# Performance work log

Hardware: AMD Instinct MI355X
Metric: run time of the kernel (lower is better)

Reference implementation:

```python
import jax, jax.numpy as jnp
from jax import lax
import numpy as np

B, N, S, K = 8, 4096, 1024, 32
D_FEAT = 64
EPS = 1e-5


def fps_idx(pts, npoint):
    # pts: [N,3] -> farthest point sampling indices [npoint] (deterministic start at 0)
    n = pts.shape[0]
    def body(i, state):
        dist, far, idxs = state
        idxs = idxs.at[i].set(far)
        d = jnp.sum((pts - pts[far]) ** 2, axis=-1)
        dist = jnp.minimum(dist, d)
        return dist, jnp.argmax(dist).astype(jnp.int32), idxs
    init = (jnp.full((n,), 1e10, pts.dtype), jnp.int32(0), jnp.zeros((npoint,), jnp.int32))
    _, _, idxs = lax.fori_loop(0, npoint, body, init)
    return idxs


def bn(x, g, b, axes, c_axis):
    # batch-norm, training mode (batch statistics), matching torch default module state
    m = jnp.mean(x, axes, keepdims=True)
    v = jnp.var(x, axes, keepdims=True)
    shape = [1] * x.ndim
    shape[c_axis] = -1
    return g.reshape(shape) * (x - m) * lax.rsqrt(v + EPS) + b.reshape(shape)


def conv1x1(x, w, b):
    # x: [B,C,S,K], w: [O,C], b: [O]
    return jnp.einsum('oc,bcsk->bosk', w, x) + b[None, :, None, None]


def setup_inputs():
    key = jax.random.key(0)
    ks = jax.random.split(key, 20)
    p = lambda k, shape: jax.random.normal(k, shape, jnp.float32) * 0.05
    inp = {
        'xyz': jax.random.normal(ks[0], (B, 3, N), jnp.float32),
        'features': jax.random.normal(ks[1], (B, D_FEAT, N), jnp.float32),
        # main MLP: 67 -> 64 -> 64 -> 128
        'w0': p(ks[2], (64, 67)), 'b0': p(ks[3], (64,)), 'g0': jnp.ones(64), 'be0': jnp.zeros(64),
        'w1': p(ks[4], (64, 64)), 'b1': p(ks[5], (64,)), 'g1': jnp.ones(64), 'be1': jnp.zeros(64),
        'w2': p(ks[6], (128, 64)), 'b2': p(ks[7], (128,)), 'g2': jnp.ones(128), 'be2': jnp.zeros(128),
        # WeightNet: 3 -> 8 -> 8 -> 16
        'ww0': p(ks[8], (8, 3)), 'wb0': p(ks[9], (8,)), 'wg0': jnp.ones(8), 'wbe0': jnp.zeros(8),
        'ww1': p(ks[10], (8, 8)), 'wb1': p(ks[11], (8,)), 'wg1': jnp.ones(8), 'wbe1': jnp.zeros(8),
        'ww2': p(ks[12], (16, 8)), 'wb2': p(ks[13], (16,)), 'wg2': jnp.ones(16), 'wbe2': jnp.zeros(16),
        # final linear 16*128 -> 128 and BN1d
        'lw': p(ks[14], (128, 16 * 128)), 'lb': p(ks[15], (128,)),
        'lg': jnp.ones(128), 'lbe': jnp.zeros(128),
    }
    return inp


def reference(xyz, features, w0, b0, g0, be0, w1, b1, g1, be1, w2, b2, g2, be2,
              ww0, wb0, wg0, wbe0, ww1, wb1, wg1, wbe1, ww2, wb2, wg2, wbe2,
              lw, lb, lg, lbe):
    xyz_t = jnp.transpose(xyz, (0, 2, 1))          # [B,N,3]
    feat_t = jnp.transpose(features, (0, 2, 1))    # [B,N,D]

    # farthest point sampling (indices non-differentiable, as in CUDA FPS)
    fidx = jax.vmap(lambda pts: fps_idx(pts, S))(lax.stop_gradient(xyz_t))  # [B,S]
    fps_xyz = jnp.take_along_axis(xyz_t, fidx[..., None], axis=1)           # [B,S,3]

    # KNN: squared distances [B,S,N], take K smallest
    d2 = (jnp.sum(fps_xyz ** 2, -1, keepdims=True)
          + jnp.sum(xyz_t ** 2, -1)[:, None, :]
          - 2.0 * jnp.einsum('bsc,bnc->bsn', fps_xyz, xyz_t))
    _, idx = lax.top_k(-lax.stop_gradient(d2), K)                            # [B,S,K]

    gather = jax.vmap(lambda src, i: src[i])
    grouped_xyz = gather(xyz_t, idx) - fps_xyz[:, :, None, :]                # [B,S,K,3]
    grouped_feat = gather(feat_t, idx)                                       # [B,S,K,D]
    nf = jnp.concatenate([grouped_xyz, grouped_feat], axis=-1)               # [B,S,K,3+D]

    nf = jnp.transpose(nf, (0, 3, 1, 2))                                     # [B,C,S,K]
    for w, b, g, be in ((w0, b0, g0, be0), (w1, b1, g1, be1), (w2, b2, g2, be2)):
        nf = jax.nn.relu(bn(conv1x1(nf, w, b), g, be, (0, 2, 3), 1))

    gx = jnp.transpose(grouped_xyz, (0, 3, 1, 2))                            # [B,3,S,K]
    wts = gx
    for w, b, g, be in ((ww0, wb0, wg0, wbe0), (ww1, wb1, wg1, wbe1), (ww2, wb2, wg2, wbe2)):
        wts = jax.nn.relu(bn(conv1x1(wts, w, b), g, be, (0, 2, 3), 1))       # [B,16,S,K]

    agg = jnp.einsum('bdsk,bcsk->bsdc', nf, wts)                             # [B,S,128,16]
    agg = agg.reshape(agg.shape[0], agg.shape[1], -1)                        # [B,S,2048] (D outer, C inner)
    lin = agg @ lw.T + lb                                                    # [B,S,128]
    lin = jnp.transpose(lin, (0, 2, 1))                                      # [B,128,S]
    out_f = jax.nn.relu(bn(lin, lg, lbe, (0, 2), 1))

    new_xyz = jnp.transpose(fps_xyz, (0, 2, 1))                              # [B,3,S]
    return (new_xyz, out_f)
```

## Files before the change

### kernel.cpp

```cpp
#include <hip/hip_runtime.h>
#include <hip/hip_bf16.h>

#define BB 8
#define NN 4096
#define SS 1024
#define KK 32
#define PP (BB*SS*KK)

typedef unsigned long long u64;
typedef unsigned int u32;
typedef unsigned short u16;
typedef float f32x2 __attribute__((ext_vector_type(2)));
typedef float f32x4 __attribute__((ext_vector_type(4)));
typedef short bf16x8 __attribute__((ext_vector_type(8)));

#define ST_Y0 0
#define ST_W0 64
#define ST_Y1 72
#define ST_W1 136
#define ST_Y2 144
#define ST_W2 272
#define ST_LIN 288

static __device__ __forceinline__ float bf2f(u32 u){ return __uint_as_float(u<<16); }
static __device__ __forceinline__ u16 f2bf(float f){ u32 u=__float_as_uint(f); return (u16)((u + 0x7FFFu + ((u>>16)&1u))>>16); }

static __device__ __forceinline__ f32x2 pk_add(f32x2 a, f32x2 b){
  f32x2 d; asm("v_pk_add_f32 %0, %1, %2" : "=v"(d) : "v"(a), "v"(b)); return d;
}
static __device__ __forceinline__ f32x2 pk_mul(f32x2 a, f32x2 b){
  f32x2 d; asm("v_pk_mul_f32 %0, %1, %2" : "=v"(d) : "v"(a), "v"(b)); return d;
}

static __device__ __forceinline__ f32x4 mfma16(bf16x8 a, bf16x8 b, f32x4 c){
  return __builtin_amdgcn_mfma_f32_16x16x32_bf16(a,b,c,0,0,0);
}

static __device__ __forceinline__ uint4 pack8(const float* v){
  uint4 r;
  r.x=(u32)f2bf(v[0])|((u32)f2bf(v[1])<<16);
  r.y=(u32)f2bf(v[2])|((u32)f2bf(v[3])<<16);
  r.z=(u32)f2bf(v[4])|((u32)f2bf(v[5])<<16);
  r.w=(u32)f2bf(v[6])|((u32)f2bf(v[7])<<16);
  return r;
}

static __device__ __forceinline__ void unp8_aff(uint4 r, const float* A, const float* C, int cb, float* o){
  o[0]=fmaxf(fmaf(bf2f(r.x&0xffffu),A[cb+0],C[cb+0]),0.f);
  o[1]=fmaxf(fmaf(bf2f(r.x>>16)    ,A[cb+1],C[cb+1]),0.f);
  o[2]=fmaxf(fmaf(bf2f(r.y&0xffffu),A[cb+2],C[cb+2]),0.f);
  o[3]=fmaxf(fmaf(bf2f(r.y>>16)    ,A[cb+3],C[cb+3]),0.f);
  o[4]=fmaxf(fmaf(bf2f(r.z&0xffffu),A[cb+4],C[cb+4]),0.f);
  o[5]=fmaxf(fmaf(bf2f(r.z>>16)    ,A[cb+5],C[cb+5]),0.f);
  o[6]=fmaxf(fmaf(bf2f(r.w&0xffffu),A[cb+6],C[cb+6]),0.f);
  o[7]=fmaxf(fmaf(bf2f(r.w>>16)    ,A[cb+7],C[cb+7]),0.f);
}

template<int CTRL, int RMASK>
static __device__ __forceinline__ u32 dppmax(u32 m){
  u32 t=(u32)__builtin_amdgcn_update_dpp(0, (int)m, CTRL, RMASK, 0xf, false);
  return t>m ? t : m;
}
template<int CTRL, int RMASK>
static __device__ __forceinline__ float dppadd1(float v){
  float t=__uint_as_float((u32)__builtin_amdgcn_update_dpp(0,(int)__float_as_uint(v),CTRL,RMASK,0xf,false));
  return v+t;
}
static __device__ __forceinline__ float dppsum(float v){
  v=dppadd1<0x111,0xf>(v);
  v=dppadd1<0x112,0xf>(v);
  v=dppadd1<0x114,0xf>(v);
  v=dppadd1<0x118,0xf>(v);
  v=dppadd1<0x142,0xa>(v);
  v=dppadd1<0x143,0xc>(v);
  return v;
}
static __device__ __forceinline__ float rl63(float v){
  return __uint_as_float((u32)__builtin_amdgcn_readlane((int)__float_as_uint(v),63));
}

__global__ __launch_bounds__(256) void k_featT(const float* __restrict__ f, float* __restrict__ ft,
    const float* __restrict__ ww0,const float* __restrict__ ww1,const float* __restrict__ ww2,
    const float* __restrict__ lw, u16* __restrict__ lwbf,
    float* __restrict__ wt0,float* __restrict__ wt1,float* __restrict__ wt2,
    float* __restrict__ statsf){
  __shared__ float tile[64][65];
  if (blockIdx.x==512){
    int t=threadIdx.x;
    for (int i=t;i<1024;i+=256) statsf[i]=0.f;
    for (int i=t;i<8*3;i+=256){ int o=i/3,k=i%3; wt0[k*8+o]=ww0[i]; }
    for (int i=t;i<8*8;i+=256){ int o=i>>3,k=i&7; wt1[k*8+o]=ww1[i]; }
    for (int i=t;i<16*8;i+=256){ int o=i>>3,k=i&7; wt2[k*16+o]=ww2[i]; }
    return;
  }
  {
    int base2=blockIdx.x*512;
    for (int i=threadIdx.x;i<512;i+=256) lwbf[base2+i]=f2bf(lw[base2+i]);
  }
  int b=blockIdx.x>>6; int n0=(blockIdx.x&63)*64;
  const float* fb=f+(size_t)b*64*NN;
  int c0=threadIdx.x>>6, nn=threadIdx.x&63;
  #pragma unroll
  for (int it=0;it<16;it++){ int c=c0+it*4; tile[c][nn]=fb[(size_t)c*NN+n0+nn]; }
  __syncthreads();
  int cc=threadIdx.x&63, n1=threadIdx.x>>6;
  float* fo=ft+((size_t)b*NN+n0)*64;
  #pragma unroll
  for (int it=0;it<16;it++){ int n=n1+it*4; fo[(size_t)n*64+cc]=tile[cc][n]; }
}

__global__ __launch_bounds__(512) void k_fps(const float* __restrict__ xyz,
                                             float* __restrict__ fpsq, float* __restrict__ outx){
  __shared__ float X[NN], Y[NN], Z[NN];
  __shared__ float QX[SS], QY[SS], QZ[SS];
  __shared__ u64 red[2][8];
  int b=blockIdx.x, t=threadIdx.x;
  const float* xb=xyz+(size_t)b*3*NN;
  for (int i=t;i<NN;i+=512){ X[i]=xb[i]; Y[i]=xb[NN+i]; Z[i]=xb[2*NN+i]; }
  __syncthreads();
  f32x2 px[4],py[4],pz[4],dd[4];
  #pragma unroll
  for (int k=0;k<4;k++){
    int i=t*8+2*k;
    px[k].x=X[i]; px[k].y=X[i+1];
    py[k].x=Y[i]; py[k].y=Y[i+1];
    pz[k].x=Z[i]; pz[k].y=Z[i+1];
    dd[k].x=1e10f; dd[k].y=1e10f;
  }
  int wv=t>>6, ln=t&63;
  int far=0;
  for (int s=0;s<SS;s++){
    float fx=X[far], fy=Y[far], fz=Z[far];
    if (t==0){ QX[s]=fx; QY[s]=fy; QZ[s]=fz; }
    f32x2 nfx, nfy, nfz;
    nfx.x=-fx; nfx.y=-fx; nfy.x=-fy; nfy.y=-fy; nfz.x=-fz; nfz.y=-fz;
    #pragma unroll
    for (int k=0;k<4;k++){
      f32x2 dx=pk_add(px[k],nfx);
      f32x2 xx=pk_mul(dx,dx);
      f32x2 dy=pk_add(py[k],nfy);
      f32x2 yy=pk_mul(dy,dy);
      f32x2 dz=pk_add(pz[k],nfz);
      f32x2 zz=pk_mul(dz,dz);
      f32x2 s1=pk_add(xx,yy);
      f32x2 d2=pk_add(s1,zz);
      dd[k].x=fminf(dd[k].x,d2.x);
      dd[k].y=fminf(dd[k].y,d2.y);
    }
    float m01=fmaxf(dd[0].x,dd[0].y), m23=fmaxf(dd[1].x,dd[1].y);
    float m45=fmaxf(dd[2].x,dd[2].y), m67=fmaxf(dd[3].x,dd[3].y);
    u32 m=__float_as_uint(fmaxf(fmaxf(m01,m23),fmaxf(m45,m67)));
    m=dppmax<0x111,0xf>(m);
    m=dppmax<0x112,0xf>(m);
    m=dppmax<0x114,0xf>(m);
    m=dppmax<0x118,0xf>(m);
    u32 r15=(u32)__builtin_amdgcn_readlane((int)m,15);
    u32 r31=(u32)__builtin_amdgcn_readlane((int)m,31);
    u32 r47=(u32)__builtin_amdgcn_readlane((int)m,47);
    u32 r63=(u32)__builtin_amdgcn_readlane((int)m,63);
    u32 ab = r15>r31 ? r15 : r31;
    u32 cd = r47>r63 ? r47 : r63;
    u32 wmax = ab>cd ? ab : cd;
    int lj=8;
    if (__float_as_uint(dd[3].y)==wmax) lj=7;
    if (__float_as_uint(dd[3].x)==wmax) lj=6;
    if (__float_as_uint(dd[2].y)==wmax) lj=5;
    if (__float_as_uint(dd[2].x)==wmax) lj=4;
    if (__float_as_uint(dd[1].y)==wmax) lj=3;
    if (__float_as_uint(dd[1].x)==wmax) lj=2;
    if (__float_as_uint(dd[0].y)==wmax) lj=1;
    if (__float_as_uint(dd[0].x)==wmax) lj=0;
    u64 ball=__ballot(lj<8);
    u32 wl=(u32)__builtin_ctzll(ball);
    int gi=t*8+lj;
    u32 widx=(u32)__builtin_amdgcn_readlane(gi,wl);
    int pb=s&1;
    if (ln==0) red[pb][wv]=((u64)wmax<<32)|(u32)(4095u-widx);
    __syncthreads();
    const double* rd=(const double*)&red[pb][0];
    double g=fmax(fmax(fmax(rd[0],rd[1]),fmax(rd[2],rd[3])),
                  fmax(fmax(rd[4],rd[5]),fmax(rd[6],rd[7])));
    far=4095-(int)(__double_as_longlong(g)&0xFFFull);
  }
  __syncthreads();
  for (int i=t;i<SS;i+=512){
    float qx=QX[i], qy=QY[i], qz=QZ[i];
    float* q=&fpsq[((size_t)b*SS+i)*3]; q[0]=qx; q[1]=qy; q[2]=qz;
    outx[b*3*SS+i]=qx; outx[b*3*SS+SS+i]=qy; outx[b*3*SS+2*SS+i]=qz;
  }
}

#define KSTR 68
__global__ __launch_bounds__(512) void k_knn(const float* __restrict__ xyz, const float* __restrict__ fpsq,
                                             int* __restrict__ kidx){
  extern __shared__ char smem[];
  float* xs=(float*)smem;
  float* ys=xs+64*KSTR;
  float* zs=ys+64*KSTR;
  float* pn=zs+64*KSTR;
  int blk=blockIdx.x; int b=blk>>7; int s0=(blk&127)*8;
  const float* xb=xyz+(size_t)b*3*NN;
  for (int i=threadIdx.x;i<NN;i+=512){
    float x=xb[i],y=xb[NN+i],z=xb[2*NN+i];
    int slot=(i>>6)*KSTR+(i&63);
    xs[slot]=x; ys[slot]=y; zs[slot]=z;
    pn[slot]=__fadd_rn(__fadd_rn(__fmul_rn(x,x),__fmul_rn(y,y)),__fmul_rn(z,z));
  }
  __syncthreads();
  int wv=threadIdx.x>>6, ln=threadIdx.x&63;
  int s=s0+wv;
  const float* q=&fpsq[((size_t)b*SS+s)*3];
  float qx=q[0],qy=q[1],qz=q[2];
  float qn=__fadd_rn(__fadd_rn(__fmul_rn(qx,qx),__fmul_rn(qy,qy)),__fmul_rn(qz,qz));
  f32x2 qxx,qyy,qzz,qnn,mtwo;
  qxx.x=qx;qxx.y=qx; qyy.x=qy;qyy.y=qy; qzz.x=qz;qzz.y=qz; qnn.x=qn;qnn.y=qn;
  mtwo.x=-2.f; mtwo.y=-2.f;
  const float4* Xp=(const float4*)(xs+ln*KSTR);
  const float4* Yp=(const float4*)(ys+ln*KSTR);
  const float4* Zp=(const float4*)(zs+ln*KSTR);
  const float4* Pp=(const float4*)(pn+ln*KSTR);
  int base=ln*64;
  u64 v[64];
  #pragma unroll
  for (int g=0;g<16;g++){
    float4 x4=Xp[g], y4=Yp[g], z4=Zp[g], p4=Pp[g];
    #pragma unroll
    for (int h=0;h<2;h++){
      f32x2 px2,py2,pz2,pn2;
      if (h==0){ px2.x=x4.x;px2.y=x4.y; py2.x=y4.x;py2.y=y4.y; pz2.x=z4.x;pz2.y=z4.y; pn2.x=p4.x;pn2.y=p4.y; }
      else     { px2.x=x4.z;px2.y=x4.w; py2.x=y4.z;py2.y=y4.w; pz2.x=z4.z;pz2.y=z4.w; pn2.x=p4.z;pn2.y=p4.w; }
      f32x2 m1=pk_mul(qxx,px2);
      f32x2 mm=pk_mul(qyy,py2);
      f32x2 a1=pk_add(m1,mm);
      f32x2 m3=pk_mul(qzz,pz2);
      f32x2 dt=pk_add(a1,m3);
      f32x2 qp=pk_add(qnn,pn2);
      f32x2 nd=pk_mul(dt,mtwo);
      f32x2 d2=pk_add(qp,nd);
      #pragma unroll
      for (int e=0;e<2;e++){
        u32 bu=__float_as_uint(e?d2.y:d2.x);
        bu = ((int)bu<0)? ~bu : (bu|0x80000000u);
        v[g*4+h*2+e]=((u64)bu<<32)|(u32)(base+g*4+h*2+e);
      }
    }
  }
  u64 cand[8];
  #pragma unroll
  for (int gg=0;gg<8;gg++){
    u64 c=v[gg*8];
    #pragma unroll
    for (int j=1;j<8;j++){ u64 x=v[gg*8+j]; c = x<c?x:c; }
    cand[gg]=c;
  }
  u64 best=cand[0];
  #pragma unroll
  for (int gg=1;gg<8;gg++){ u64 x=cand[gg]; best = x<best?x:best; }
  int my=0;
  #pragma unroll 1
  for (int r=0;r<KK;r++){
    u64 w=best;
    #pragma unroll
    for (int m=1;m<64;m<<=1){ u64 o=__shfl_xor(w,m,64); w = o<w?o:w; }
    if (ln==r) my=(int)(w&0xFFFull);
    if (best==w){
      #pragma unroll
      for (int gg=0;gg<8;gg++){
        if (cand[gg]==w){
          u64 c=~0ull;
          #pragma unroll
          for (int j=0;j<8;j++){ u64 x=v[gg*8+j]; x = x>w ? x : ~0ull; c = x<c?x:c; }
          cand[gg]=c;
        }
      }
      u64 nb=cand[0];
      #pragma unroll
      for (int gg=1;gg<8;gg++){ u64 x=cand[gg]; nb = x<nb?x:nb; }
      best=nb;
    }
  }
  if (ln<KK) kidx[(((size_t)b*SS+s)<<5)+ln]=my;
}

__global__ __launch_bounds__(256) void k_l0(const float* __restrict__ xyz, const float* __restrict__ ft,
    const float* __restrict__ fpsq, const int* __restrict__ kidx,
    const float* __restrict__ w0, const float* __restrict__ wt0,
    u16* __restrict__ y0, float* __restrict__ wl0, float* __restrict__ statsf){
  __shared__ u16 Bw[64*72];
  __shared__ float gt[256][4];
  __shared__ int jt[256];
  __shared__ float pS[4][64], pQ[4][64];
  __shared__ float pWS[4][8], pWQ[4][8];
  int t=threadIdx.x; int wv=t>>6, ln=t&63;
  int p=blockIdx.x*256+t;
  int b=p>>15;
  int site=p>>5;
  int j=kidx[p];
  const float* xb=xyz+(size_t)b*3*NN;
  const float* q=fpsq+(size_t)site*3;
  float gx=xb[j]-q[0], gy=xb[NN+j]-q[1], gz=xb[2*NN+j]-q[2];
  gt[t][0]=gx; gt[t][1]=gy; gt[t][2]=gz; gt[t][3]=0.f; jt[t]=j;
  for (int i=t;i<4096;i+=256){ int col=i>>6,k=i&63; Bw[col*72+k]=f2bf(w0[col*67+3+k]); }
  __syncthreads();
  float wxc[4],wyc[4],wzc[4];
  #pragma unroll
  for (int n=0;n<4;n++){
    int c=n*16+(ln&15);
    wxc[n]=w0[c*67+0]; wyc[n]=w0[c*67+1]; wzc[n]=w0[c*67+2];
  }
  float sS[4]={0,0,0,0}, sQ[4]={0,0,0,0};
  int base=wv*64;
  #pragma unroll 1
  for (int rs=0;rs<4;rs++){
    int lrow=base+rs*16+(ln&15);
    int jr=jt[lrow];
    const float* fp=ft+((size_t)b*NN+jr)*64 + (ln>>4)*8;
    float4 fa=*(const float4*)fp, fb4=*(const float4*)(fp+4);
    float4 fc=*(const float4*)(fp+32), fd=*(const float4*)(fp+36);
    float va[8]={fa.x,fa.y,fa.z,fa.w,fb4.x,fb4.y,fb4.z,fb4.w};
    float vb[8]={fc.x,fc.y,fc.z,fc.w,fd.x,fd.y,fd.z,fd.w};
    bf16x8 a0,a1;
    #pragma unroll
    for (int e=0;e<8;e++){ ((u16*)&a0)[e]=(short)f2bf(va[e]); ((u16*)&a1)[e]=(short)f2bf(vb[e]); }
    int r0=base+rs*16+(ln>>4)*4;
    float4 g0v4=*(const float4*)&gt[r0+0][0];
    float4 g1v4=*(const float4*)&gt[r0+1][0];
    float4 g2v4=*(const float4*)&gt[r0+2][0];
    float4 g3v4=*(const float4*)&gt[r0+3][0];
    float gxr[4]={g0v4.x,g1v4.x,g2v4.x,g3v4.x};
    float gyr[4]={g0v4.y,g1v4.y,g2v4.y,g3v4.y};
    float gzr[4]={g0v4.z,g1v4.z,g2v4.z,g3v4.z};
    int pr=blockIdx.x*256+base+rs*16;
    #pragma unroll
    for (int n=0;n<4;n++){
      const u16* bp=&Bw[(size_t)(n*16+(ln&15))*72 + (ln>>4)*8];
      bf16x8 b0=*(const bf16x8*)bp;
      bf16x8 b1=*(const bf16x8*)(bp+32);
      f32x4 acc;
      #pragma unroll
      for (int i=0;i<4;i++) acc[i]=fmaf(gxr[i],wxc[n],fmaf(gyr[i],wyc[n],gzr[i]*wzc[n]));
      acc=mfma16(a0,b0,acc);
      acc=mfma16(a1,b1,acc);
      #pragma unroll
      for (int i=0;i<4;i++){
        int row=(ln>>4)*4+i;
        y0[(size_t)(pr+row)*64 + n*16 + (ln&15)]=f2bf(acc[i]);
        sS[n]+=acc[i]; sQ[n]=fmaf(acc[i],acc[i],sQ[n]);
      }
    }
  }
  #pragma unroll
  for (int n=0;n<4;n++){
    sS[n]+=__shfl_xor(sS[n],16,64); sS[n]+=__shfl_xor(sS[n],32,64);
    sQ[n]+=__shfl_xor(sQ[n],16,64); sQ[n]+=__shfl_xor(sQ[n],32,64);
  }
  if (ln<16){
    #pragma unroll
    for (int n=0;n<4;n++){ pS[wv][n*16+ln]=sS[n]; pQ[wv][n*16+ln]=sQ[n]; }
  }
  float wa[8];
  #pragma unroll
  for (int o=0;o<8;o++) wa[o]=fmaf(gx,wt0[o],fmaf(gy,wt0[8+o],gz*wt0[16+o]));
  float4* wr=(float4*)(wl0+(size_t)p*8);
  wr[0]=make_float4(wa[0],wa[1],wa[2],wa[3]);
  wr[1]=make_float4(wa[4],wa[5],wa[6],wa[7]);
  float wS[8],wQ[8];
  #pragma unroll
  for (int o=0;o<8;o++){
    wS[o]=rl63(dppsum(wa[o]));
    wQ[o]=rl63(dppsum(wa[o]*wa[o]));
  }
  if (ln==0){
    #pragma unroll
    for (int o=0;o<8;o++){ pWS[wv][o]=wS[o]; pWQ[wv][o]=wQ[o]; }
  }
  __syncthreads();
  if (t<64){
    float S=pS[0][t]+pS[1][t]+pS[2][t]+pS[3][t];
    float Q=pQ[0][t]+pQ[1][t]+pQ[2][t]+pQ[3][t];
    atomicAdd(&statsf[2*(ST_Y0+t)],S); atomicAdd(&statsf[2*(ST_Y0+t)+1],Q);
  } else if (t<72){
    int c=t-64;
    float S=pWS[0][c]+pWS[1][c]+pWS[2][c]+pWS[3][c];
    float Q=pWQ[0][c]+pWQ[1][c]+pWQ[2][c]+pWQ[3][c];
    atomicAdd(&statsf[2*(ST_W0+c)],S); atomicAdd(&statsf[2*(ST_W0+c)+1],Q);
  }
}

__global__ __launch_bounds__(256) void k_l1(const u16* __restrict__ y0, const float* __restrict__ wl0,
    const float* __restrict__ w1, const float* __restrict__ wt1,
    const float* __restrict__ statsf,
    const float* __restrict__ g0v, const float* __restrict__ be0v,
    const float* __restrict__ wg0v, const float* __restrict__ wbe0v,
    u16* __restrict__ y1, float* __restrict__ wl1, float* __restrict__ statso){
  __shared__ float A0[64],C0[64],AW[8],CW[8];
  __shared__ u16 Bw[64*72];
  __shared__ u16 Atile[4][16*72];
  __shared__ float pS[4][64], pQ[4][64];
  __shared__ float pWS[4][8], pWQ[4][8];
  int t=threadIdx.x; int wv=t>>6, ln=t&63;
  if (t<64){
    float sm=statsf[(ST_Y0+t)*2], sq=statsf[(ST_Y0+t)*2+1];
    float mean=sm*(1.f/PP), var=fmaxf(sq*(1.f/PP)-mean*mean,0.f);
    float a=g0v[t]*rsqrtf(var+1e-5f); A0[t]=a; C0[t]=be0v[t]-mean*a;
  } else if (t<72){
    int c=t-64;
    float sm=statsf[(ST_W0+c)*2], sq=statsf[(ST_W0+c)*2+1];
    float mean=sm*(1.f/PP), var=fmaxf(sq*(1.f/PP)-mean*mean,0.f);
    float a=wg0v[c]*rsqrtf(var+1e-5f); AW[c]=a; CW[c]=wbe0v[c]-mean*a;
  }
  for (int i=t;i<4096;i+=256){ Bw[(i>>6)*72+(i&63)]=f2bf(w1[i]); }
  __syncthreads();
  bf16x8 bfr[4][2];
  #pragma unroll
  for (int n=0;n<4;n++){
    const u16* bp=&Bw[(size_t)(n*16+(ln&15))*72 + (ln>>4)*8];
    bfr[n][0]=*(const bf16x8*)bp;
    bfr[n][1]=*(const bf16x8*)(bp+32);
  }
  float sS[4]={0,0,0,0}, sQ[4]={0,0,0,0};
  int p0=blockIdx.x*256 + wv*64;
  u16* At=Atile[wv];
  #pragma unroll 1
  for (int rs=0;rs<4;rs++){
    int pr=p0+rs*16;
    {
      const u16* ysrc=y0+(size_t)pr*64 + ln*16;
      uint4 raw0=*(const uint4*)ysrc;
      uint4 raw1=*(const uint4*)(ysrc+8);
      int row=ln>>2, cb=(ln&3)*16;
      float tmp[8];
      unp8_aff(raw0,A0,C0,cb,tmp);
      *(uint4*)&At[row*72+cb]=pack8(tmp);
      unp8_aff(raw1,A0,C0,cb+8,tmp);
      *(uint4*)&At[row*72+cb+8]=pack8(tmp);
    }
    const u16* ap=&At[(ln&15)*72 + (ln>>4)*8];
    bf16x8 a0=*(const bf16x8*)ap;
    bf16x8 a1=*(const bf16x8*)(ap+32);
    #pragma unroll
    for (int n=0;n<4;n++){
      f32x4 acc={0.f,0.f,0.f,0.f};
      acc=mfma16(a0,bfr[n][0],acc);
      acc=mfma16(a1,bfr[n][1],acc);
      #pragma unroll
      for (int i=0;i<4;i++){
        int row=(ln>>4)*4+i;
        y1[(size_t)(pr+row)*64 + n*16 + (ln&15)]=f2bf(acc[i]);
        sS[n]+=acc[i]; sQ[n]=fmaf(acc[i],acc[i],sQ[n]);
      }
    }
  }
  #pragma unroll
  for (int n=0;n<4;n++){
    sS[n]+=__shfl_xor(sS[n],16,64); sS[n]+=__shfl_xor(sS[n],32,64);
    sQ[n]+=__shfl_xor(sQ[n],16,64); sQ[n]+=__shfl_xor(sQ[n],32,64);
  }
  if (ln<16){
    #pragma unroll
    for (int n=0;n<4;n++){ pS[wv][n*16+ln]=sS[n]; pQ[wv][n*16+ln]=sQ[n]; }
  }
  int p=blockIdx.x*256+t;
  const float4* wvp=(const float4*)(wl0+(size_t)p*8);
  float4 v0=wvp[0], v1=wvp[1];
  float wi[8]={v0.x,v0.y,v0.z,v0.w,v1.x,v1.y,v1.z,v1.w};
  float wo[8];
  #pragma unroll
  for (int o=0;o<8;o++) wo[o]=0.f;
  #pragma unroll
  for (int k=0;k<8;k++){
    float xr=fmaxf(fmaf(wi[k],AW[k],CW[k]),0.f);
    #pragma unroll
    for (int o=0;o<8;o++) wo[o]=fmaf(xr,wt1[k*8+o],wo[o]);
  }
  float4* wr=(float4*)(wl1+(size_t)p*8);
  wr[0]=make_float4(wo[0],wo[1],wo[2],wo[3]);
  wr[1]=make_float4(wo[4],wo[5],wo[6],wo[7]);
  float wS[8],wQ[8];
  #pragma unroll
  for (int o=0;o<8;o++){
    wS[o]=rl63(dppsum(wo[o]));
    wQ[o]=rl63(dppsum(wo[o]*wo[o]));
  }
  if (ln==0){
    #pragma unroll
    for (int o=0;o<8;o++){ pWS[wv][o]=wS[o]; pWQ[wv][o]=wQ[o]; }
  }
  __syncthreads();
  if (t<64){
    float S=pS[0][t]+pS[1][t]+pS[2][t]+pS[3][t];
    float Q=pQ[0][t]+pQ[1][t]+pQ[2][t]+pQ[3][t];
    atomicAdd(&statso[2*(ST_Y1+t)],S); atomicAdd(&statso[2*(ST_Y1+t)+1],Q);
  } else if (t<72){
    int c=t-64;
    float S=pWS[0][c]+pWS[1][c]+pWS[2][c]+pWS[3][c];
    float Q=pWQ[0][c]+pWQ[1][c]+pWQ[2][c]+pWQ[3][c];
    atomicAdd(&statso[2*(ST_W1+c)],S); atomicAdd(&statso[2*(ST_W1+c)+1],Q);
  }
}

__global__ __launch_bounds__(256) void k_l2(const u16* __restrict__ y1, const float* __restrict__ wl1,
    const float* __restrict__ w2, const float* __restrict__ wt2,
    const float* __restrict__ statsf,
    const float* __restrict__ g1v, const float* __restrict__ be1v,
    const float* __restrict__ wg1v, const float* __restrict__ wbe1v,
    u16* __restrict__ y2, float* __restrict__ wl2, float* __restrict__ statso){
  __shared__ float A1[64],C1[64],AW[8],CW[8];
  __shared__ u16 Bw[128*72];
  __shared__ u16 Atile[4][16*72];
  __shared__ float pS[4][128], pQ[4][128];
  __shared__ float pWS[4][16], pWQ[4][16];
  int t=threadIdx.x; int wv=t>>6, ln=t&63;
  if (t<64){
    float sm=statsf[(ST_Y1+t)*2], sq=statsf[(ST_Y1+t)*2+1];
    float mean=sm*(1.f/PP), var=fmaxf(sq*(1.f/PP)-mean*mean,0.f);
    float a=g1v[t]*rsqrtf(var+1e-5f); A1[t]=a; C1[t]=be1v[t]-mean*a;
  } else if (t<72){
    int c=t-64;
    float sm=statsf[(ST_W1+c)*2], sq=statsf[(ST_W1+c)*2+1];
    float mean=sm*(1.f/PP), var=fmaxf(sq*(1.f/PP)-mean*mean,0.f);
    float a=wg1v[c]*rsqrtf(var+1e-5f); AW[c]=a; CW[c]=wbe1v[c]-mean*a;
  }
  for (int i=t;i<8192;i+=256){ Bw[(i>>6)*72+(i&63)]=f2bf(w2[i]); }
  __syncthreads();
  float sS[8]={0,0,0,0,0,0,0,0}, sQ[8]={0,0,0,0,0,0,0,0};
  int p0=blockIdx.x*256 + wv*64;
  u16* At=Atile[wv];
  #pragma unroll 1
  for (int rs=0;rs<4;rs++){
    int pr=p0+rs*16;
    {
      const u16* ysrc=y1+(size_t)pr*64 + ln*16;
      uint4 raw0=*(const uint4*)ysrc;
      uint4 raw1=*(const uint4*)(ysrc+8);
      int row=ln>>2, cb=(ln&3)*16;
      float tmp[8];
      unp8_aff(raw0,A1,C1,cb,tmp);
      *(uint4*)&At[row*72+cb]=pack8(tmp);
      unp8_aff(raw1,A1,C1,cb+8,tmp);
      *(uint4*)&At[row*72+cb+8]=pack8(tmp);
    }
    const u16* ap=&At[(ln&15)*72 + (ln>>4)*8];
    bf16x8 a0=*(const bf16x8*)ap;
    bf16x8 a1=*(const bf16x8*)(ap+32);
    #pragma unroll
    for (int n=0;n<8;n++){
      const u16* bp=&Bw[(size_t)(n*16+(ln&15))*72 + (ln>>4)*8];
      bf16x8 b0=*(const bf16x8*)bp;
      bf16x8 b1=*(const bf16x8*)(bp+32);
      f32x4 acc={0.f,0.f,0.f,0.f};
      acc=mfma16(a0,b0,acc);
      acc=mfma16(a1,b1,acc);
      #pragma unroll
      for (int i=0;i<4;i++){
        int row=(ln>>4)*4+i;
        y2[(size_t)(pr+row)*128 + n*16 + (ln&15)]=f2bf(acc[i]);
        sS[n]+=acc[i]; sQ[n]=fmaf(acc[i],acc[i],sQ[n]);
      }
    }
  }
  #pragma unroll
  for (int n=0;n<8;n++){
    sS[n]+=__shfl_xor(sS[n],16,64); sS[n]+=__shfl_xor(sS[n],32,64);
    sQ[n]+=__shfl_xor(sQ[n],16,64); sQ[n]+=__shfl_xor(sQ[n],32,64);
  }
  if (ln<16){
    #pragma unroll
    for (int n=0;n<8;n++){ pS[wv][n*16+ln]=sS[n]; pQ[wv][n*16+ln]=sQ[n]; }
  }
  int p=blockIdx.x*256+t;
  const float4* wvp=(const float4*)(wl1+(size_t)p*8);
  float4 v0=wvp[0], v1=wvp[1];
  float wi[8]={v0.x,v0.y,v0.z,v0.w,v1.x,v1.y,v1.z,v1.w};
  float wo[16];
  #pragma unroll
  for (int o=0;o<16;o++) wo[o]=0.f;
  #pragma unroll
  for (int k=0;k<8;k++){
    float xr=fmaxf(fmaf(wi[k],AW[k],CW[k]),0.f);
    #pragma unroll
    for (int o=0;o<16;o++) wo[o]=fmaf(xr,wt2[k*16+o],wo[o]);
  }
  float4* wr=(float4*)(wl2+(size_t)p*16);
  wr[0]=make_float4(wo[0],wo[1],wo[2],wo[3]);
  wr[1]=make_float4(wo[4],wo[5],wo[6],wo[7]);
  wr[2]=make_float4(wo[8],wo[9],wo[10],wo[11]);
  wr[3]=make_float4(wo[12],wo[13],wo[14],wo[15]);
  float wS[16],wQ[16];
  #pragma unroll
  for (int o=0;o<16;o++){
    wS[o]=rl63(dppsum(wo[o]));
    wQ[o]=rl63(dppsum(wo[o]*wo[o]));
  }
  if (ln==0){
    #pragma unroll
    for (int o=0;o<16;o++){ pWS[wv][o]=wS[o]; pWQ[wv][o]=wQ[o]; }
  }
  __syncthreads();
  if (t<128){
    float S=pS[0][t]+pS[1][t]+pS[2][t]+pS[3][t];
    float Q=pQ[0][t]+pQ[1][t]+pQ[2][t]+pQ[3][t];
    atomicAdd(&statso[2*(ST_Y2+t)],S); atomicAdd(&statso[2*(ST_Y2+t)+1],Q);
  } else if (t<144){
    int c=t-128;
    float S=pWS[0][c]+pWS[1][c]+pWS[2][c]+pWS[3][c];
    float Q=pWQ[0][c]+pWQ[1][c]+pWQ[2][c]+pWQ[3][c];
    atomicAdd(&statso[2*(ST_W2+c)],S); atomicAdd(&statso[2*(ST_W2+c)+1],Q);
  }
}

__global__ __launch_bounds__(256) void k_agg(const u16* __restrict__ y2, const float* __restrict__ wl2,
    const float* __restrict__ statsf,
    const float* __restrict__ g2v, const float* __restrict__ be2v,
    const float* __restrict__ wg2v, const float* __restrict__ wbe2v,
    u16* __restrict__ agg){
  __shared__ float A2[128],C2[128],AW[16],CW[16];
  __shared__ float nf[32*128];
  __shared__ float wt[32*16];
  int site=blockIdx.x; int t=threadIdx.x;
  if (t<128){
    float sm=statsf[(ST_Y2+t)*2], sq=statsf[(ST_Y2+t)*2+1];
    float mean=sm*(1.f/PP), var=fmaxf(sq*(1.f/PP)-mean*mean,0.f);
    float a=g2v[t]*rsqrtf(var+1e-5f); A2[t]=a; C2[t]=be2v[t]-mean*a;
  } else if (t<144){
    int c=t-128;
    float sm=statsf[(ST_W2+c)*2], sq=statsf[(ST_W2+c)*2+1];
    float mean=sm*(1.f/PP), var=fmaxf(sq*(1.f/PP)-mean*mean,0.f);
    float a=wg2v[c]*rsqrtf(var+1e-5f); AW[c]=a; CW[c]=wbe2v[c]-mean*a;
  }
  __syncthreads();
  const uint4* src=(const uint4*)(y2+(size_t)site*32*128);
  #pragma unroll
  for (int it=0;it<2;it++){
    int idx=t+it*256;
    uint4 r=src[idx];
    int base=(idx*8)&127; int kq=(idx*8)>>7;
    unp8_aff(r,A2,C2,base,&nf[kq*128+base]);
  }
  #pragma unroll
  for (int it=0;it<2;it++){
    int i=t+it*256;
    float x=wl2[(size_t)site*512+i]; int c=i&15;
    wt[i]=fmaxf(fmaf(x,AW[c],CW[c]),0.f);
  }
  __syncthreads();
  int d=t>>1, cb=(t&1)*8;
  float acc[8];
  #pragma unroll
  for (int e=0;e<8;e++) acc[e]=0.f;
  #pragma unroll 4
  for (int kq=0;kq<32;kq++){
    float nv=nf[kq*128+d];
    #pragma unroll
    for (int e=0;e<8;e++) acc[e]=fmaf(nv,wt[kq*16+cb+e],acc[e]);
  }
  ((uint4*)(agg+(size_t)site*2048))[t]=pack8(acc);
}

__global__ __launch_bounds__(256) void k_lin(const u16* __restrict__ agg, const u16* __restrict__ lwbf,
                                             float* __restrict__ lin, float* __restrict__ outst){
  __shared__ float pS[4][32], pQ[4][32];
  int t=threadIdx.x; int wv=t>>6, ln=t&63;
  int s0=blockIdx.x*16;
  const u16* arow=agg+(size_t)(s0+(ln&15))*2048 + (ln>>4)*8;
  const u16* b0p=lwbf+(size_t)(wv*32+(ln&15))*2048 + (ln>>4)*8;
  const u16* b1p=b0p + (size_t)16*2048;
  f32x4 acc0={0.f,0.f,0.f,0.f}, acc1={0.f,0.f,0.f,0.f};
  #pragma unroll 4
  for (int kb=0;kb<2048;kb+=32){
    bf16x8 a=*(const bf16x8*)(arow+kb);
    bf16x8 b0=*(const bf16x8*)(b0p+kb);
    bf16x8 b1=*(const bf16x8*)(b1p+kb);
    acc0=mfma16(a,b0,acc0);
    acc1=mfma16(a,b1,acc1);
  }
  float sS0=0.f,sQ0=0.f,sS1=0.f,sQ1=0.f;
  #pragma unroll
  for (int i=0;i<4;i++){
    int row=(ln>>4)*4+i;
    lin[(size_t)(s0+row)*128 + wv*32 + (ln&15)]=acc0[i];
    lin[(size_t)(s0+row)*128 + wv*32 + 16 + (ln&15)]=acc1[i];
    sS0+=acc0[i]; sQ0=fmaf(acc0[i],acc0[i],sQ0);
    sS1+=acc1[i]; sQ1=fmaf(acc1[i],acc1[i],sQ1);
  }
  sS0+=__shfl_xor(sS0,16,64); sS0+=__shfl_xor(sS0,32,64);
  sQ0+=__shfl_xor(sQ0,16,64); sQ0+=__shfl_xor(sQ0,32,64);
  sS1+=__shfl_xor(sS1,16,64); sS1+=__shfl_xor(sS1,32,64);
  sQ1+=__shfl_xor(sQ1,16,64); sQ1+=__shfl_xor(sQ1,32,64);
  if (ln<16){ pS[wv][ln]=sS0; pS[wv][16+ln]=sS1; pQ[wv][ln]=sQ0; pQ[wv][16+ln]=sQ1; }
  __syncthreads();
  if (t<128){
    float S=pS[t>>5][t&31], Q=pQ[t>>5][t&31];
    atomicAdd(&outst[2*t],S); atomicAdd(&outst[2*t+1],Q);
  }
}

__global__ __launch_bounds__(256) void k_out(const float* __restrict__ lin, const float* __restrict__ statsf,
    const float* __restrict__ lg, const float* __restrict__ lbe, float* __restrict__ outf){
  int t=blockIdx.x*256+threadIdx.x;
  int s4=(t&255)*4; int o=(t>>8)&127; int b=t>>15;
  float sm=statsf[(ST_LIN+o)*2], sq=statsf[(ST_LIN+o)*2+1];
  float mean=sm*(1.f/8192.f), var=fmaxf(sq*(1.f/8192.f)-mean*mean,0.f);
  float a=lg[o]*rsqrtf(var+1e-5f), cc=lbe[o]-mean*a;
  float v0=lin[((size_t)b*SS+s4+0)*128+o];
  float v1=lin[((size_t)b*SS+s4+1)*128+o];
  float v2=lin[((size_t)b*SS+s4+2)*128+o];
  float v3=lin[((size_t)b*SS+s4+3)*128+o];
  float4 r=make_float4(fmaxf(fmaf(v0,a,cc),0.f),fmaxf(fmaf(v1,a,cc),0.f),
                       fmaxf(fmaf(v2,a,cc),0.f),fmaxf(fmaf(v3,a,cc),0.f));
  *(float4*)(outf+((size_t)b*128+o)*SS+s4)=r;
}

extern "C" void kernel_launch(void* const* d_in, const int* in_sizes, int n_in,
                              void* d_out, int out_size, void* d_ws, size_t ws_size,
                              hipStream_t stream){
  (void)in_sizes;(void)n_in;(void)out_size;(void)ws_size;
  const float* xyz =(const float*)d_in[0];
  const float* feat=(const float*)d_in[1];
  const float* w0=(const float*)d_in[2];  const float* g0=(const float*)d_in[4];  const float* be0=(const float*)d_in[5];
  const float* w1=(const float*)d_in[6];  const float* g1=(const float*)d_in[8];  const float* be1=(const float*)d_in[9];
  const float* w2=(const float*)d_in[10]; const float* g2=(const float*)d_in[12]; const float* be2=(const float*)d_in[13];
  const float* ww0=(const float*)d_in[14]; const float* wg0=(const float*)d_in[16]; const float* wbe0=(const float*)d_in[17];
  const float* ww1=(const float*)d_in[18]; const float* wg1=(const float*)d_in[20]; const float* wbe1=(const float*)d_in[21];
  const float* ww2=(const float*)d_in[22]; const float* wg2=(const float*)d_in[24]; const float* wbe2=(const float*)d_in[25];
  const float* lw=(const float*)d_in[26]; const float* lg=(const float*)d_in[28]; const float* lbe=(const float*)d_in[29];
  float* out=(float*)d_out;
  char* ws=(char*)d_ws;

  size_t cur=0;
  auto alloc=[&](size_t bytes)->size_t{ cur=(cur+255)&~(size_t)255; size_t o=cur; cur+=bytes; return o; };
  size_t o_stats=alloc(4096);
  size_t o_wt0 =alloc(3*8*4);
  size_t o_wt1 =alloc(8*8*4);
  size_t o_wt2 =alloc(8*16*4);
  size_t o_lwbf=alloc((size_t)128*2048*2);
  size_t o_fpsq=alloc((size_t)BB*SS*3*4);
  size_t o_kidx=alloc((size_t)PP*4);
  size_t o_ft  =alloc((size_t)BB*NN*64*4);
  size_t o_y0  =alloc((size_t)PP*64*2);
  size_t o_y1  =alloc((size_t)PP*64*2);
  size_t o_y2  =alloc((size_t)PP*128*2);
  size_t o_wl0 =alloc((size_t)PP*8*4);
  size_t o_wl1 =alloc((size_t)PP*8*4);
  size_t o_wl2 =alloc((size_t)PP*16*4);
  size_t o_agg =alloc((size_t)8192*2048*2);
  size_t o_lin =alloc((size_t)8192*128*4);

  float* statsf=(float*)(ws+o_stats);
  float* wt0=(float*)(ws+o_wt0); float* wt1=(float*)(ws+o_wt1); float* wt2=(float*)(ws+o_wt2);
  u16* lwbf=(u16*)(ws+o_lwbf);
  float* fpsq=(float*)(ws+o_fpsq); int* kidx=(int*)(ws+o_kidx);
  float* ft=(float*)(ws+o_ft);
  u16* y0=(u16*)(ws+o_y0); u16* y1=(u16*)(ws+o_y1); u16* y2=(u16*)(ws+o_y2);
  float* wl0=(float*)(ws+o_wl0); float* wl1=(float*)(ws+o_wl1); float* wl2=(float*)(ws+o_wl2);
  u16* agg=(u16*)(ws+o_agg); float* lin=(float*)(ws+o_lin);

  size_t knn_smem = (size_t)4*64*KSTR*4;

  hipLaunchKernelGGL(k_featT,dim3(513),dim3(256),0,stream,feat,ft,
                     ww0,ww1,ww2,lw,lwbf,wt0,wt1,wt2,statsf);
  hipLaunchKernelGGL(k_fps,dim3(BB),dim3(512),0,stream,xyz,fpsq,out);
  hipLaunchKernelGGL(k_knn,dim3(1024),dim3(512),knn_smem,stream,xyz,fpsq,kidx);
  hipLaunchKernelGGL(k_l0,dim3(PP/256),dim3(256),0,stream,xyz,ft,fpsq,kidx,w0,wt0,y0,wl0,statsf);
  hipLaunchKernelGGL(k_l1,dim3(PP/256),dim3(256),0,stream,y0,wl0,w1,wt1,statsf,g0,be0,wg0,wbe0,y1,wl1,statsf);
  hipLaunchKernelGGL(k_l2,dim3(PP/256),dim3(256),0,stream,y1,wl1,w2,wt2,statsf,g1,be1,wg1,wbe1,y2,wl2,statsf);
  hipLaunchKernelGGL(k_agg,dim3(8192),dim3(256),0,stream,y2,wl2,statsf,g2,be2,wg2,wbe2,agg);
  hipLaunchKernelGGL(k_lin,dim3(512),dim3(256),0,stream,agg,lwbf,lin,statsf+2*ST_LIN);
  hipLaunchKernelGGL(k_out,dim3(1024),dim3(256),0,stream,lin,statsf,lg,lbe,out+BB*3*SS);
}
```

Before: 1.096 ms.

## Fuse aggregation into linear GEMM via LDS and merge feature transpose into KNN

Aggregation now runs inside the linear kernel. Each block computes the bf16 agg rows for 16 sites into shared memory and feeds them straight to the MFMA GEMM, so the 32MB agg buffer is never written to or read back from global memory. Separately, the feature transpose, weight prep and stats zeroing move into extra blocks of the KNN launch, which removes one launch and lets them overlap with KNN. In exchange, the fused kernel has only 512 blocks, and each loops serially over 16 sites with reads from y2 that are no longer coalesced, which may reduce parallelism for the aggregation work.

```diff
diff --git a/kernel.cpp b/kernel.cpp
--- a/kernel.cpp
+++ b/kernel.cpp
@@ -77,36 +77,6 @@
 }
 static __device__ __forceinline__ float rl63(float v){
   return __uint_as_float((u32)__builtin_amdgcn_readlane((int)__float_as_uint(v),63));
-}
-
-__global__ __launch_bounds__(256) void k_featT(const float* __restrict__ f, float* __restrict__ ft,
-    const float* __restrict__ ww0,const float* __restrict__ ww1,const float* __restrict__ ww2,
-    const float* __restrict__ lw, u16* __restrict__ lwbf,
-    float* __restrict__ wt0,float* __restrict__ wt1,float* __restrict__ wt2,
-    float* __restrict__ statsf){
-  __shared__ float tile[64][65];
-  if (blockIdx.x==512){
-    int t=threadIdx.x;
-    for (int i=t;i<1024;i+=256) statsf[i]=0.f;
-    for (int i=t;i<8*3;i+=256){ int o=i/3,k=i%3; wt0[k*8+o]=ww0[i]; }
-    for (int i=t;i<8*8;i+=256){ int o=i>>3,k=i&7; wt1[k*8+o]=ww1[i]; }
-    for (int i=t;i<16*8;i+=256){ int o=i>>3,k=i&7; wt2[k*16+o]=ww2[i]; }
-    return;
-  }
-  {
-    int base2=blockIdx.x*512;
-    for (int i=threadIdx.x;i<512;i+=256) lwbf[base2+i]=f2bf(lw[base2+i]);
-  }
-  int b=blockIdx.x>>6; int n0=(blockIdx.x&63)*64;
-  const float* fb=f+(size_t)b*64*NN;
-  int c0=threadIdx.x>>6, nn=threadIdx.x&63;
-  #pragma unroll
-  for (int it=0;it<16;it++){ int c=c0+it*4; tile[c][nn]=fb[(size_t)c*NN+n0+nn]; }
-  __syncthreads();
-  int cc=threadIdx.x&63, n1=threadIdx.x>>6;
-  float* fo=ft+((size_t)b*NN+n0)*64;
-  #pragma unroll
-  for (int it=0;it<16;it++){ int n=n1+it*4; fo[(size_t)n*64+cc]=tile[cc][n]; }
 }
 
 __global__ __launch_bounds__(512) void k_fps(const float* __restrict__ xyz,
@@ -191,23 +161,56 @@
 }
 
 #define KSTR 68
-__global__ __launch_bounds__(512) void k_knn(const float* __restrict__ xyz, const float* __restrict__ fpsq,
-                                             int* __restrict__ kidx){
+__global__ __launch_bounds__(512) void k_knnft(const float* __restrict__ xyz, const float* __restrict__ fpsq,
+    int* __restrict__ kidx,
+    const float* __restrict__ f, float* __restrict__ ft,
+    const float* __restrict__ ww0,const float* __restrict__ ww1,const float* __restrict__ ww2,
+    const float* __restrict__ lw, u16* __restrict__ lwbf,
+    float* __restrict__ wt0,float* __restrict__ wt1,float* __restrict__ wt2,
+    float* __restrict__ statsf){
   extern __shared__ char smem[];
+  int blk=blockIdx.x; int t=threadIdx.x;
+  if (blk>=1024){
+    if (blk==1280){
+      for (int i=t;i<1024;i+=512) statsf[i]=0.f;
+      for (int i=t;i<8*3;i+=512){ int o=i/3,k=i%3; wt0[k*8+o]=ww0[i]; }
+      for (int i=t;i<8*8;i+=512){ int o=i>>3,k=i&7; wt1[k*8+o]=ww1[i]; }
+      for (int i=t;i<16*8;i+=512){ int o=i>>3,k=i&7; wt2[k*16+o]=ww2[i]; }
+      return;
+    }
+    {
+      int base2=(blk-1024)*1024;
+      for (int i=t;i<1024;i+=512) lwbf[base2+i]=f2bf(lw[base2+i]);
+    }
+    float (*tile)[64][65]=(float(*)[64][65])smem;
+    int sub=t>>8, tt=t&255;
+    int tileIdx=(blk-1024)*2+sub;
+    int b=tileIdx>>6; int n0=(tileIdx&63)*64;
+    const float* fb=f+(size_t)b*64*NN;
+    int c0=tt>>6, nn=tt&63;
+    #pragma unroll
+    for (int it=0;it<16;it++){ int c=c0+it*4; tile[sub][c][nn]=fb[(size_t)c*NN+n0+nn]; }
+    __syncthreads();
+    int cc=tt&63, n1=tt>>6;
+    float* fo=ft+((size_t)b*NN+n0)*64;
+    #pragma unroll
+    for (int it=0;it<16;it++){ int n=n1+it*4; fo[(size_t)n*64+cc]=tile[sub][cc][n]; }
+    return;
+  }
   float* xs=(float*)smem;
   float* ys=xs+64*KSTR;
   float* zs=ys+64*KSTR;
   float* pn=zs+64*KSTR;
-  int blk=blockIdx.x; int b=blk>>7; int s0=(blk&127)*8;
+  int b=blk>>7; int s0=(blk&127)*8;
   const float* xb=xyz+(size_t)b*3*NN;
-  for (int i=threadIdx.x;i<NN;i+=512){
+  for (int i=t;i<NN;i+=512){
     float x=xb[i],y=xb[NN+i],z=xb[2*NN+i];
     int slot=(i>>6)*KSTR+(i&63);
     xs[slot]=x; ys[slot]=y; zs[slot]=z;
     pn[slot]=__fadd_rn(__fadd_rn(__fmul_rn(x,x),__fmul_rn(y,y)),__fmul_rn(z,z));
   }
   __syncthreads();
-  int wv=threadIdx.x>>6, ln=threadIdx.x&63;
+  int wv=t>>6, ln=t&63;
   int s=s0+wv;
   const float* q=&fpsq[((size_t)b*SS+s)*3];
   float qx=q[0],qy=q[1],qz=q[2];
@@ -609,15 +612,17 @@
   }
 }
 
-__global__ __launch_bounds__(256) void k_agg(const u16* __restrict__ y2, const float* __restrict__ wl2,
+__global__ __launch_bounds__(256) void k_agglin(const u16* __restrict__ y2, const float* __restrict__ wl2,
     const float* __restrict__ statsf,
     const float* __restrict__ g2v, const float* __restrict__ be2v,
     const float* __restrict__ wg2v, const float* __restrict__ wbe2v,
-    u16* __restrict__ agg){
+    const u16* __restrict__ lwbf, float* __restrict__ lin, float* __restrict__ outst){
   __shared__ float A2[128],C2[128],AW[16],CW[16];
-  __shared__ float nf[32*128];
   __shared__ float wt[32*16];
-  int site=blockIdx.x; int t=threadIdx.x;
+  __shared__ u16 aggt[16][2056];
+  __shared__ float pS[4][32], pQ[4][32];
+  int t=threadIdx.x; int wv=t>>6, ln=t&63;
+  int s0=blockIdx.x*16;
   if (t<128){
     float sm=statsf[(ST_Y2+t)*2], sq=statsf[(ST_Y2+t)*2+1];
     float mean=sm*(1.f/PP), var=fmaxf(sq*(1.f/PP)-mean*mean,0.f);
@@ -629,40 +634,32 @@
     float a=wg2v[c]*rsqrtf(var+1e-5f); AW[c]=a; CW[c]=wbe2v[c]-mean*a;
   }
   __syncthreads();
-  const uint4* src=(const uint4*)(y2+(size_t)site*32*128);
-  #pragma unroll
-  for (int it=0;it<2;it++){
-    int idx=t+it*256;
-    uint4 r=src[idx];
-    int base=(idx*8)&127; int kq=(idx*8)>>7;
-    unp8_aff(r,A2,C2,base,&nf[kq*128+base]);
-  }
-  #pragma unroll
-  for (int it=0;it<2;it++){
-    int i=t+it*256;
-    float x=wl2[(size_t)site*512+i]; int c=i&15;
-    wt[i]=fmaxf(fmaf(x,AW[c],CW[c]),0.f);
-  }
-  __syncthreads();
   int d=t>>1, cb=(t&1)*8;
-  float acc[8];
-  #pragma unroll
-  for (int e=0;e<8;e++) acc[e]=0.f;
-  #pragma unroll 4
-  for (int kq=0;kq<32;kq++){
-    float nv=nf[kq*128+d];
-    #pragma unroll
-    for (int e=0;e<8;e++) acc[e]=fmaf(nv,wt[kq*16+cb+e],acc[e]);
-  }
-  ((uint4*)(agg+(size_t)site*2048))[t]=pack8(acc);
-}
-
-__global__ __launch_bounds__(256) void k_lin(const u16* __restrict__ agg, const u16* __restrict__ lwbf,
-                                             float* __restrict__ lin, float* __restrict__ outst){
-  __shared__ float pS[4][32], pQ[4][32];
-  int t=threadIdx.x; int wv=t>>6, ln=t&63;
-  int s0=blockIdx.x*16;
-  const u16* arow=agg+(size_t)(s0+(ln&15))*2048 + (ln>>4)*8;
+  float a2d=A2[d], c2d=C2[d];
+  #pragma unroll 1
+  for (int si=0; si<16; si++){
+    int site=s0+si;
+    #pragma unroll
+    for (int it=0; it<2; it++){
+      int i=t+it*256;
+      float x=wl2[(size_t)site*512+i]; int c=i&15;
+      wt[i]=fmaxf(fmaf(x,AW[c],CW[c]),0.f);
+    }
+    __syncthreads();
+    float acc[8];
+    #pragma unroll
+    for (int e=0;e<8;e++) acc[e]=0.f;
+    const u16* ys=y2+(size_t)site*4096;
+    #pragma unroll 4
+    for (int kq=0;kq<32;kq++){
+      float nv=fmaxf(fmaf(bf2f((u32)ys[kq*128+d]),a2d,c2d),0.f);
+      #pragma unroll
+      for (int e=0;e<8;e++) acc[e]=fmaf(nv,wt[kq*16+cb+e],acc[e]);
+    }
+    *(uint4*)&aggt[si][d*16+cb]=pack8(acc);
+    __syncthreads();
+  }
+  const u16* arow=&aggt[ln&15][(ln>>4)*8];
   const u16* b0p=lwbf+(size_t)(wv*32+(ln&15))*2048 + (ln>>4)*8;
   const u16* b1p=b0p + (size_t)16*2048;
   f32x4 acc0={0.f,0.f,0.f,0.f}, acc1={0.f,0.f,0.f,0.f};
@@ -743,7 +740,6 @@
   size_t o_wl0 =alloc((size_t)PP*8*4);
   size_t o_wl1 =alloc((size_t)PP*8*4);
   size_t o_wl2 =alloc((size_t)PP*16*4);
-  size_t o_agg =alloc((size_t)8192*2048*2);
   size_t o_lin =alloc((size_t)8192*128*4);
 
   float* statsf=(float*)(ws+o_stats);
@@ -753,18 +749,16 @@
   float* ft=(float*)(ws+o_ft);
   u16* y0=(u16*)(ws+o_y0); u16* y1=(u16*)(ws+o_y1); u16* y2=(u16*)(ws+o_y2);
   float* wl0=(float*)(ws+o_wl0); float* wl1=(float*)(ws+o_wl1); float* wl2=(float*)(ws+o_wl2);
-  u16* agg=(u16*)(ws+o_agg); float* lin=(float*)(ws+o_lin);
+  float* lin=(float*)(ws+o_lin);
 
   size_t knn_smem = (size_t)4*64*KSTR*4;
 
-  hipLaunchKernelGGL(k_featT,dim3(513),dim3(256),0,stream,feat,ft,
-                     ww0,ww1,ww2,lw,lwbf,wt0,wt1,wt2,statsf);
   hipLaunchKernelGGL(k_fps,dim3(BB),dim3(512),0,stream,xyz,fpsq,out);
-  hipLaunchKernelGGL(k_knn,dim3(1024),dim3(512),knn_smem,stream,xyz,fpsq,kidx);
+  hipLaunchKernelGGL(k_knnft,dim3(1281),dim3(512),knn_smem,stream,xyz,fpsq,kidx,
+                     feat,ft,ww0,ww1,ww2,lw,lwbf,wt0,wt1,wt2,statsf);
   hipLaunchKernelGGL(k_l0,dim3(PP/256),dim3(256),0,stream,xyz,ft,fpsq,kidx,w0,wt0,y0,wl0,statsf);
   hipLaunchKernelGGL(k_l1,dim3(PP/256),dim3(256),0,stream,y0,wl0,w1,wt1,statsf,g0,be0,wg0,wbe0,y1,wl1,statsf);
   hipLaunchKernelGGL(k_l2,dim3(PP/256),dim3(256),0,stream,y1,wl1,w2,wt2,statsf,g1,be1,wg1,wbe1,y2,wl2,statsf);
-  hipLaunchKernelGGL(k_agg,dim3(8192),dim3(256),0,stream,y2,wl2,statsf,g2,be2,wg2,wbe2,agg);
-  hipLaunchKernelGGL(k_lin,dim3(512),dim3(256),0,stream,agg,lwbf,lin,statsf+2*ST_LIN);
+  hipLaunchKernelGGL(k_agglin,dim3(512),dim3(256),0,stream,y2,wl2,statsf,g2,be2,wg2,wbe2,lwbf,lin,statsf+2*ST_LIN);
   hipLaunchKernelGGL(k_out,dim3(1024),dim3(256),0,stream,lin,statsf,lg,lbe,out+BB*3*SS);
 }
```

Result: no change. 1.077 ms (-1.7%).
